# Performance work log

Measured on AMD Instinct MI355X. Metric: run time of the kernel, lower is better.

## Reference

```python
import jax, jax.numpy as jnp
import numpy as np

B, C, N = 64, 81, 8732


def setup_inputs() -> dict:
    key = jax.random.key(0)
    k1, k2, k3, k4, k5 = jax.random.split(key, 5)
    ploc = jax.random.normal(k1, (B, 4, N), dtype=jnp.float32)
    plabel = jax.random.normal(k2, (B, C, N), dtype=jnp.float32)
    # gloc: uniform, shifted positive so gwh/dwh log is well-defined
    gloc = jax.random.uniform(k3, (B, 4, N), dtype=jnp.float32) * 0.9 + 0.05
    glabel = jax.random.randint(k4, (B, N), 0, C, dtype=jnp.int64)
    # default boxes: keep widths/heights bounded away from 0
    dboxes = jax.random.uniform(k5, (1, 4, N), dtype=jnp.float32) * 0.9 + 0.1
    return {"ploc": ploc, "plabel": plabel, "gloc": gloc, "glabel": glabel, "dboxes": dboxes}


def _smooth_l1(x):
    ax = jnp.abs(x)
    return jnp.where(ax < 1.0, 0.5 * ax * ax, ax - 0.5)


def reference(ploc, plabel, gloc, glabel, dboxes):
    mask = glabel > 0                       # [B, N] positive anchors
    num_pos = mask.sum(axis=1)              # [B]

    # encode ground-truth boxes as offsets relative to default boxes
    dxy, dwh = dboxes[:, :2, :], dboxes[:, 2:, :]
    gxy = (gloc[:, :2, :] - dxy) / dwh
    gwh = jnp.log(gloc[:, 2:, :] / dwh)
    goff = jnp.concatenate([gxy, gwh], axis=1)  # [B, 4, N]

    # localization loss: smooth L1 summed over coords, masked to positives
    loc = _smooth_l1(ploc - goff).sum(axis=1)   # [B, N]
    loc_loss = (mask * loc).sum(axis=1)         # [B]

    # per-anchor cross entropy
    logp = jax.nn.log_softmax(plabel, axis=1)   # [B, C, N]
    closs = -jnp.take_along_axis(logp, glabel[:, None, :], axis=1)[:, 0, :]  # [B, N]

    # hard negative mining via rank (double argsort, descending)
    con_neg = jnp.where(mask, 0.0, closs)
    con_idx = jnp.argsort(-con_neg, axis=1)
    con_rank = jnp.argsort(con_idx, axis=1)
    neg_num = jnp.minimum(3 * num_pos, N)[:, None]
    neg_mask = con_rank < neg_num
    con_loss = (closs * (mask.astype(jnp.float32) + neg_mask.astype(jnp.float32))).sum(axis=1)

    total = loc_loss + con_loss
    num_mask = (num_pos > 0).astype(jnp.float32)
    npos = jnp.clip(num_pos.astype(jnp.float32), 1e-6)
    return ((total * num_mask) / npos).mean()
```

## Files before the change

kernel.cpp:

```cpp
#include <hip/hip_runtime.h>
#include <math.h>

#define BATCH 64
#define NCLS  81
#define NANCH 8732
#define NG    (NANCH / 4)
#define BLK   256
#define BPB   ((NG + BLK - 1) / BLK)

__device__ inline float smooth_l1(float d) {
    float a = fabsf(d);
    return (a < 1.f) ? 0.5f * a * a : a - 0.5f;
}

__global__ __launch_bounds__(256) void k_main(
    const float* __restrict__ ploc, const float* __restrict__ plabel,
    const float* __restrict__ gloc, const int* __restrict__ glabel,
    const float* __restrict__ dboxes, float4* __restrict__ partials)
{
    const int b   = blockIdx.x / BPB;
    const int gid = (blockIdx.x % BPB) * BLK + threadIdx.x;

    float l_loc = 0.f, l_posc = 0.f, l_negc = 0.f;
    int   l_cnt = 0;

    if (gid < NG) {
        const float4* pl4 = (const float4*)(plabel + (size_t)b * NCLS * NANCH);
        const int4*   gp  = (const int4*)(glabel + (size_t)b * NANCH);
        const int4    gi  = gp[gid];
        const int g[4] = {gi.x, gi.y, gi.z, gi.w};

        float m[4], s[4], xg[4];
#pragma unroll
        for (int i = 0; i < 4; ++i) { m[i] = -INFINITY; s[i] = 0.f; xg[i] = 0.f; }

        for (int c = 0; c < NCLS; ++c) {
            float4 xv = pl4[c * NG + gid];
            float x[4] = {xv.x, xv.y, xv.z, xv.w};
#pragma unroll
            for (int i = 0; i < 4; ++i) {
                float nm = fmaxf(m[i], x[i]);
                float e  = __expf(fminf(m[i], x[i]) - nm);
                s[i] = (x[i] > m[i]) ? s[i] * e + 1.f : s[i] + e;
                m[i] = nm;
                if (c == g[i]) xg[i] = x[i];
            }
        }

        const float4* pploc = (const float4*)(ploc + (size_t)b * 4 * NANCH);
        const float4* pgloc = (const float4*)(gloc + (size_t)b * 4 * NANCH);
        const float4* pdb   = (const float4*)dboxes;
        float P[4][4], G[4][4], D[4][4];
#pragma unroll
        for (int ch = 0; ch < 4; ++ch) {
            float4 p = pploc[ch * NG + gid];
            float4 q = pgloc[ch * NG + gid];
            float4 d = pdb[ch * NG + gid];
            P[ch][0]=p.x; P[ch][1]=p.y; P[ch][2]=p.z; P[ch][3]=p.w;
            G[ch][0]=q.x; G[ch][1]=q.y; G[ch][2]=q.z; G[ch][3]=q.w;
            D[ch][0]=d.x; D[ch][1]=d.y; D[ch][2]=d.z; D[ch][3]=d.w;
        }

#pragma unroll
        for (int i = 0; i < 4; ++i) {
            float gx = (G[0][i] - D[0][i]) / D[2][i];
            float gy = (G[1][i] - D[1][i]) / D[3][i];
            float gw = __logf(G[2][i] / D[2][i]);
            float gh = __logf(G[3][i] / D[3][i]);
            float loc_i = smooth_l1(P[0][i] - gx) + smooth_l1(P[1][i] - gy)
                        + smooth_l1(P[2][i] - gw) + smooth_l1(P[3][i] - gh);
            float closs = m[i] + __logf(s[i]) - xg[i];
            bool  mk = g[i] > 0;
            l_loc  += mk ? loc_i : 0.f;
            l_posc += mk ? closs : 0.f;
            l_negc += mk ? 0.f : closs;
            l_cnt  += mk ? 1 : 0;
        }
    }

#pragma unroll
    for (int off = 32; off; off >>= 1) {
        l_loc  += __shfl_down(l_loc, off);
        l_posc += __shfl_down(l_posc, off);
        l_negc += __shfl_down(l_negc, off);
        l_cnt  += __shfl_down(l_cnt, off);
    }
    __shared__ float sl[4], sp[4], sn[4];
    __shared__ int   sc[4];
    const int wave = threadIdx.x >> 6, lane = threadIdx.x & 63;
    if (lane == 0) { sl[wave] = l_loc; sp[wave] = l_posc; sn[wave] = l_negc; sc[wave] = l_cnt; }
    __syncthreads();
    if (threadIdx.x == 0) {
        float a = 0.f, p = 0.f, n = 0.f; int ct = 0;
#pragma unroll
        for (int w = 0; w < 4; ++w) { a += sl[w]; p += sp[w]; n += sn[w]; ct += sc[w]; }
        partials[blockIdx.x] = make_float4(a, p, n, (float)ct);
    }
}

__device__ float closs_at(const float* __restrict__ plabel, int b, int n, int g) {
    const float* p = plabel + (size_t)b * NCLS * NANCH + n;
    float m = -INFINITY, s = 0.f, xg = 0.f;
    for (int c = 0; c < NCLS; ++c) {
        float x = p[(size_t)c * NANCH];
        float nm = fmaxf(m, x);
        float e  = __expf(fminf(m, x) - nm);
        s = (x > m) ? s * e + 1.f : s + e;
        m = nm;
        if (c == g) xg = x;
    }
    return m + __logf(s) - xg;
}

__global__ __launch_bounds__(256) void k_fin(
    const float* __restrict__ plabel, const int* __restrict__ glabel,
    const float4* __restrict__ partials, float* __restrict__ out)
{
    const int tid = threadIdx.x;
    __shared__ float s_contrib[BATCH];
    __shared__ float s_loc[BATCH], s_posc[BATCH], s_negc[BATCH];
    __shared__ int   s_np[BATCH], s_cold[BATCH];
    __shared__ unsigned int hist[256];
    __shared__ unsigned int s_bucket;
    __shared__ long long s_rnext;
    __shared__ float rs[4], rc[4];

    if (tid < BATCH) {
        const int b = tid;
        float loc = 0.f, pc = 0.f, nc = 0.f, cf = 0.f;
#pragma unroll
        for (int j = 0; j < BPB; ++j) {
            float4 v = partials[b * BPB + j];
            loc += v.x; pc += v.y; nc += v.z; cf += v.w;
        }
        const int np = (int)(cf + 0.5f);
        s_loc[b] = loc; s_posc[b] = pc; s_negc[b] = nc; s_np[b] = np;
        s_contrib[b] = 0.f;
        s_cold[b] = 0;
        if (np > 0) {
            long long K = 3LL * np; if (K > NANCH) K = NANCH;
            const int nn = NANCH - np;
            if ((long long)nn <= K) {
                long long extra = K - nn;
                if (extra >= np) {
                    float total = loc + 2.f * pc + nc;
                    s_contrib[b] = total / fmaxf((float)np, 1e-6f) * (1.f / BATCH);
                } else {
                    s_cold[b] = 1;
                }
            } else {
                s_cold[b] = 2;
            }
        }
    }
    __syncthreads();

    for (int b = 0; b < BATCH; ++b) {
        const int mode = s_cold[b];
        if (mode == 0) continue;
        const int np = s_np[b];
        long long K = 3LL * np; if (K > NANCH) K = NANCH;
        const int nn = NANCH - np;

        if (mode == 1) {
            long long extra = K - nn;
            if (tid < 64) {
                long long cnt = 0; float sum = 0.f;
                for (int base = 0; base < NANCH; base += 64) {
                    int n = base + tid;
                    int gl = (n < NANCH) ? glabel[(size_t)b * NANCH + n] : 0;
                    bool p = gl > 0;
                    unsigned long long bal = __ballot(p);
                    int r = __popcll(bal & ((1ull << tid) - 1ull));
                    if (p && (cnt + r) < extra) sum += closs_at(plabel, b, n, gl);
                    cnt += (long long)__popcll(bal);
                }
#pragma unroll
                for (int off = 32; off; off >>= 1) sum += __shfl_down(sum, off);
                if (tid == 0) {
                    float total = s_loc[b] + s_posc[b] + (s_negc[b] + sum);
                    s_contrib[b] = total / fmaxf((float)np, 1e-6f) * (1.f / BATCH);
                }
            }
        } else {
            unsigned int prefix = 0;
            long long r = K;
            for (int level = 3; level >= 0; --level) {
                const int shift = level * 8;
                hist[tid] = 0u;
                __syncthreads();
                const unsigned int pmask =
                    (level == 3) ? 0u : (0xFFFFFFFFu << ((level + 1) * 8));
                for (int n = tid; n < NANCH; n += 256) {
                    int gl = glabel[(size_t)b * NANCH + n];
                    float v = (gl > 0) ? 0.f : fmaxf(closs_at(plabel, b, n, gl), 0.f);
                    unsigned int bits = __float_as_uint(v);
                    if ((bits & pmask) == (prefix & pmask))
                        atomicAdd(&hist[(bits >> shift) & 255u], 1u);
                }
                __syncthreads();
                if (tid == 0) {
                    long long acc_c = 0; int bsel = 0;
                    for (int i = 255; i >= 0; --i) {
                        if (acc_c + (long long)hist[i] >= r) { bsel = i; break; }
                        acc_c += hist[i];
                    }
                    s_bucket = (unsigned int)bsel;
                    s_rnext  = r - acc_c;
                }
                __syncthreads();
                prefix |= (s_bucket << shift);
                r = s_rnext;
                __syncthreads();
            }
            const float T = __uint_as_float(prefix);
            float lsum = 0.f, lcnt = 0.f;
            for (int n = tid; n < NANCH; n += 256) {
                int gl = glabel[(size_t)b * NANCH + n];
                float v = (gl > 0) ? 0.f : fmaxf(closs_at(plabel, b, n, gl), 0.f);
                if (v > T) { lsum += v; lcnt += 1.f; }
            }
#pragma unroll
            for (int off = 32; off; off >>= 1) {
                lsum += __shfl_down(lsum, off);
                lcnt += __shfl_down(lcnt, off);
            }
            const int wave = tid >> 6, lane = tid & 63;
            if (lane == 0) { rs[wave] = lsum; rc[wave] = lcnt; }
            __syncthreads();
            if (tid == 0) {
                float gsum = 0.f, gcnt = 0.f;
#pragma unroll
                for (int w = 0; w < 4; ++w) { gsum += rs[w]; gcnt += rc[w]; }
                float sel = gsum + ((float)K - gcnt) * T;
                float total = s_loc[b] + s_posc[b] + sel;
                s_contrib[b] = total / fmaxf((float)np, 1e-6f) * (1.f / BATCH);
            }
        }
        __syncthreads();
    }
    __syncthreads();

    if (tid == 0) {
        float acc = 0.f;
#pragma unroll
        for (int b = 0; b < BATCH; ++b) acc += s_contrib[b];
        out[0] = acc;
    }
}

extern "C" void kernel_launch(void* const* d_in, const int* in_sizes, int n_in,
                              void* d_out, int out_size, void* d_ws, size_t ws_size,
                              hipStream_t stream) {
    const float* ploc   = (const float*)d_in[0];
    const float* plabel = (const float*)d_in[1];
    const float* gloc   = (const float*)d_in[2];
    const int*   glabel = (const int*)d_in[3];
    const float* dboxes = (const float*)d_in[4];
    float* out = (float*)d_out;
    float4* partials = (float4*)d_ws;

    hipLaunchKernelGGL(k_main, dim3(BATCH * BPB), dim3(256), 0, stream,
                       ploc, plabel, gloc, glabel, dboxes, partials);
    hipLaunchKernelGGL(k_fin, dim3(1), dim3(256), 0, stream,
                       plabel, glabel, partials, out);
}
```

Before: 290.7 us.

## Split class softmax into three independent accumulators with register prefetch

The online log-sum-exp over the 81 classes now runs as three independent streams, one per class modulo 3, and they are merged at the end. This breaks the serial dependency chain on the running max and sum. Each loop trip also loads the next three class rows before working on the current ones, and the box loads are moved ahead of the class loop, so more memory requests are in flight per thread. In exchange the kernel uses more registers, which may reduce occupancy, and the last trip issues a redundant reload.

After: 286.9 us. No clear change (-1.3%).

```diff
diff --git a/kernel.cpp b/kernel.cpp
--- a/kernel.cpp
+++ b/kernel.cpp
@@ -7,10 +7,24 @@
 #define NG    (NANCH / 4)
 #define BLK   256
 #define BPB   ((NG + BLK - 1) / BLK)
+#define CTRIP (NCLS / 3)
 
 __device__ inline float smooth_l1(float d) {
     float a = fabsf(d);
     return (a < 1.f) ? 0.5f * a * a : a - 0.5f;
+}
+
+__device__ inline void upd(float m[4], float s[4], float xg[4],
+                           const float4 xv, int c, const int g[4]) {
+    const float x[4] = {xv.x, xv.y, xv.z, xv.w};
+#pragma unroll
+    for (int i = 0; i < 4; ++i) {
+        float nm = fmaxf(m[i], x[i]);
+        float e  = __expf(fminf(m[i], x[i]) - nm);
+        s[i] = (x[i] > m[i]) ? s[i] * e + 1.f : s[i] + e;
+        m[i] = nm;
+        xg[i] = (c == g[i]) ? x[i] : xg[i];
+    }
 }
 
 __global__ __launch_bounds__(256) void k_main(
@@ -25,51 +39,71 @@
     int   l_cnt = 0;
 
     if (gid < NG) {
-        const float4* pl4 = (const float4*)(plabel + (size_t)b * NCLS * NANCH);
-        const int4*   gp  = (const int4*)(glabel + (size_t)b * NANCH);
-        const int4    gi  = gp[gid];
-        const int g[4] = {gi.x, gi.y, gi.z, gi.w};
-
-        float m[4], s[4], xg[4];
-#pragma unroll
-        for (int i = 0; i < 4; ++i) { m[i] = -INFINITY; s[i] = 0.f; xg[i] = 0.f; }
-
-        for (int c = 0; c < NCLS; ++c) {
-            float4 xv = pl4[c * NG + gid];
-            float x[4] = {xv.x, xv.y, xv.z, xv.w};
-#pragma unroll
-            for (int i = 0; i < 4; ++i) {
-                float nm = fmaxf(m[i], x[i]);
-                float e  = __expf(fminf(m[i], x[i]) - nm);
-                s[i] = (x[i] > m[i]) ? s[i] * e + 1.f : s[i] + e;
-                m[i] = nm;
-                if (c == g[i]) xg[i] = x[i];
-            }
-        }
-
         const float4* pploc = (const float4*)(ploc + (size_t)b * 4 * NANCH);
         const float4* pgloc = (const float4*)(gloc + (size_t)b * 4 * NANCH);
         const float4* pdb   = (const float4*)dboxes;
-        float P[4][4], G[4][4], D[4][4];
+        float4 Pv[4], Gv[4], Dv[4];
 #pragma unroll
         for (int ch = 0; ch < 4; ++ch) {
-            float4 p = pploc[ch * NG + gid];
-            float4 q = pgloc[ch * NG + gid];
-            float4 d = pdb[ch * NG + gid];
-            P[ch][0]=p.x; P[ch][1]=p.y; P[ch][2]=p.z; P[ch][3]=p.w;
-            G[ch][0]=q.x; G[ch][1]=q.y; G[ch][2]=q.z; G[ch][3]=q.w;
-            D[ch][0]=d.x; D[ch][1]=d.y; D[ch][2]=d.z; D[ch][3]=d.w;
-        }
-
+            Pv[ch] = pploc[ch * NG + gid];
+            Gv[ch] = pgloc[ch * NG + gid];
+            Dv[ch] = pdb[ch * NG + gid];
+        }
+        const int4 gi = ((const int4*)(glabel + (size_t)b * NANCH))[gid];
+        const int g[4] = {gi.x, gi.y, gi.z, gi.w};
+
+        const float4* pl4 = (const float4*)(plabel + (size_t)b * NCLS * NANCH);
+
+        float m0[4], s0[4], xg0[4], m1[4], s1[4], xg1[4], m2[4], s2[4], xg2[4];
 #pragma unroll
         for (int i = 0; i < 4; ++i) {
+            m0[i] = m1[i] = m2[i] = -INFINITY;
+            s0[i] = s1[i] = s2[i] = 0.f;
+            xg0[i] = xg1[i] = xg2[i] = 0.f;
+        }
+
+        float4 nx0 = pl4[0 * NG + gid];
+        float4 nx1 = pl4[1 * NG + gid];
+        float4 nx2 = pl4[2 * NG + gid];
+
+        for (int cc = 0; cc < CTRIP; ++cc) {
+            const float4 a0 = nx0, a1 = nx1, a2 = nx2;
+            const int cb = (cc < CTRIP - 1) ? 3 * (cc + 1) : 3 * cc;
+            nx0 = pl4[(cb + 0) * NG + gid];
+            nx1 = pl4[(cb + 1) * NG + gid];
+            nx2 = pl4[(cb + 2) * NG + gid];
+            upd(m0, s0, xg0, a0, 3 * cc + 0, g);
+            upd(m1, s1, xg1, a1, 3 * cc + 1, g);
+            upd(m2, s2, xg2, a2, 3 * cc + 2, g);
+        }
+
+        const float P[4][4] = {{Pv[0].x,Pv[0].y,Pv[0].z,Pv[0].w},
+                               {Pv[1].x,Pv[1].y,Pv[1].z,Pv[1].w},
+                               {Pv[2].x,Pv[2].y,Pv[2].z,Pv[2].w},
+                               {Pv[3].x,Pv[3].y,Pv[3].z,Pv[3].w}};
+        const float G[4][4] = {{Gv[0].x,Gv[0].y,Gv[0].z,Gv[0].w},
+                               {Gv[1].x,Gv[1].y,Gv[1].z,Gv[1].w},
+                               {Gv[2].x,Gv[2].y,Gv[2].z,Gv[2].w},
+                               {Gv[3].x,Gv[3].y,Gv[3].z,Gv[3].w}};
+        const float D[4][4] = {{Dv[0].x,Dv[0].y,Dv[0].z,Dv[0].w},
+                               {Dv[1].x,Dv[1].y,Dv[1].z,Dv[1].w},
+                               {Dv[2].x,Dv[2].y,Dv[2].z,Dv[2].w},
+                               {Dv[3].x,Dv[3].y,Dv[3].z,Dv[3].w}};
+
+#pragma unroll
+        for (int i = 0; i < 4; ++i) {
+            float M = fmaxf(fmaxf(m0[i], m1[i]), m2[i]);
+            float S = s0[i] * __expf(m0[i] - M)
+                    + s1[i] * __expf(m1[i] - M)
+                    + s2[i] * __expf(m2[i] - M);
+            float closs = M + __logf(S) - (xg0[i] + xg1[i] + xg2[i]);
+
             float gx = (G[0][i] - D[0][i]) / D[2][i];
             float gy = (G[1][i] - D[1][i]) / D[3][i];
             float gw = __logf(G[2][i] / D[2][i]);
             float gh = __logf(G[3][i] / D[3][i]);
             float loc_i = smooth_l1(P[0][i] - gx) + smooth_l1(P[1][i] - gy)
                         + smooth_l1(P[2][i] - gw) + smooth_l1(P[3][i] - gh);
-            float closs = m[i] + __logf(s[i]) - xg[i];
             bool  mk = g[i] > 0;
             l_loc  += mk ? loc_i : 0.f;
             l_posc += mk ? closs : 0.f;
```
